# Kernel optimization log

Measured on AMD Instinct MI355X. Metric: run time of the kernel, lower is better.

Reference implementation:

```python
import jax, jax.numpy as jnp
import numpy as np

B, L, D, K, NFFT = 4, 8192, 768, 24, 16384


def setup_inputs() -> dict:
    key = jax.random.key(0)
    k1, k2, k3, k4 = jax.random.split(key, 4)
    x = jax.random.normal(k1, (B, L, D), dtype=jnp.float32)
    phi = jax.random.normal(k2, (L, K), dtype=jnp.float32) * 0.1
    M_inputs = jax.random.normal(k3, (D, D), dtype=jnp.float32) * 0.02
    M_filters = jax.random.normal(k4, (K, D), dtype=jnp.float32) * 0.02
    return {"x": x, "phi": phi, "M_inputs": M_inputs, "M_filters": M_filters, "n": NFFT}


def _convolve_approx(u, v, n):
    # u: (B, L, D) projected inputs; v: (L, D) projected filters (per-channel kernels)
    bsz, seq_len, d = u.shape
    sgn = jnp.where(jnp.arange(seq_len) % 2 == 0, 1.0, -1.0).astype(u.dtype)[None, :, None]  # (1,L,1)
    V = jnp.fft.rfft(v.astype(jnp.float32), n=n, axis=0)[None, :, :, None]  # (1,F,D,1)
    U = jnp.stack([u, u * sgn], axis=-1).astype(jnp.float32)  # (B,L,D,2): [plus, sign-flipped]
    Uf = jnp.fft.rfft(U, n=n, axis=1)  # (B,F,D,2)
    conv = jnp.fft.irfft(V * Uf, n=n, axis=1)[:, :seq_len]  # (B,L,D,2)
    U_plus = conv[..., 0]
    U_minus = conv[..., 1] * sgn
    return U_plus, U_minus


def reference(x, phi, M_inputs, M_filters, n):
    x_proj = x @ M_inputs          # (B,L,D)
    phi_proj = phi @ M_filters     # (L,D)
    spectral_plus, spectral_minus = _convolve_approx(x_proj, phi_proj, n)
    return spectral_plus + spectral_minus
```

## Files before the change

kernel.cpp:

```cpp
#include <hip/hip_runtime.h>
#include <stdint.h>

#define B_SZ 4
#define L_SEQ 8192
#define D_CH 768
#define K_F 24
#define NFFT2 8192
#define LDS_BYTES 69632
#define GEMM_LDS 98304

typedef __attribute__((ext_vector_type(4))) float f32x4;
typedef __attribute__((ext_vector_type(8))) __bf16 bf16x8;

__device__ __forceinline__ uint32_t f2bf1(float f) {
  uint32_t u = __float_as_uint(f);
  return (u + 0x7fffu + ((u >> 16) & 1u)) >> 16;
}
__device__ __forceinline__ uint32_t packbf2(float lo, float hi) {
  return f2bf1(lo) | (f2bf1(hi) << 16);
}
__device__ __forceinline__ float2 unpackbf2(uint32_t v) {
  return float2{__uint_as_float(v << 16), __uint_as_float(v & 0xffff0000u)};
}
__device__ __forceinline__ float2 cmulf(float2 a, float2 b) {
  return float2{a.x * b.x - a.y * b.y, a.x * b.y + a.y * b.x};
}
__device__ __forceinline__ uint32_t pkbf(float lo, float hi) {
  uint32_t r;
  asm("v_cvt_pk_bf16_f32 %0, %1, %2" : "=v"(r) : "v"(lo), "v"(hi));
  return r;
}

__global__ __launch_bounds__(256) void k_mit(const float* __restrict__ Mi,
                                             uint16_t* __restrict__ MiT) {
  int i = blockIdx.x * 256 + threadIdx.x;
  int n = i / 768, e = i - n * 768;
  MiT[i] = (uint16_t)f2bf1(Mi[e * 768 + n]);
}

template <int S>
__device__ __forceinline__ void dft8(float2* x) {
  const float C = 0.70710678118654752f;
  float2 t0{x[0].x + x[4].x, x[0].y + x[4].y}, t1{x[0].x - x[4].x, x[0].y - x[4].y};
  float2 t2{x[2].x + x[6].x, x[2].y + x[6].y}, t3{x[2].x - x[6].x, x[2].y - x[6].y};
  float2 t4{x[1].x + x[5].x, x[1].y + x[5].y}, t5{x[1].x - x[5].x, x[1].y - x[5].y};
  float2 t6{x[3].x + x[7].x, x[3].y + x[7].y}, t7{x[3].x - x[7].x, x[3].y - x[7].y};
  float2 t3r = (S < 0) ? float2{t3.y, -t3.x} : float2{-t3.y, t3.x};
  float2 t7r = (S < 0) ? float2{t7.y, -t7.x} : float2{-t7.y, t7.x};
  float2 e0{t0.x + t2.x, t0.y + t2.y}, e2{t0.x - t2.x, t0.y - t2.y};
  float2 e1{t1.x + t3r.x, t1.y + t3r.y}, e3{t1.x - t3r.x, t1.y - t3r.y};
  float2 o0{t4.x + t6.x, t4.y + t6.y}, o2{t4.x - t6.x, t4.y - t6.y};
  float2 o1{t5.x + t7r.x, t5.y + t7r.y}, o3{t5.x - t7r.x, t5.y - t7r.y};
  float2 o1r = (S < 0) ? float2{C * (o1.x + o1.y), C * (o1.y - o1.x)}
                       : float2{C * (o1.x - o1.y), C * (o1.y + o1.x)};
  float2 o2r = (S < 0) ? float2{o2.y, -o2.x} : float2{-o2.y, o2.x};
  float2 o3r = (S < 0) ? float2{C * (o3.y - o3.x), -C * (o3.x + o3.y)}
                       : float2{-C * (o3.x + o3.y), C * (o3.x - o3.y)};
  x[0] = float2{e0.x + o0.x, e0.y + o0.y};
  x[4] = float2{e0.x - o0.x, e0.y - o0.y};
  x[1] = float2{e1.x + o1r.x, e1.y + o1r.y};
  x[5] = float2{e1.x - o1r.x, e1.y - o1r.y};
  x[2] = float2{e2.x + o2r.x, e2.y + o2r.y};
  x[6] = float2{e2.x - o2r.x, e2.y - o2r.y};
  x[3] = float2{e3.x + o3r.x, e3.y + o3r.y};
  x[7] = float2{e3.x - o3r.x, e3.y - o3r.y};
}

template <int LH, int S, int NT>
__device__ __forceinline__ void pass_r8(float2* a, int tid) {
  constexpr int h = 1 << LH;
  constexpr int st = h + (h >> 4);
  const float ang = (S < 0 ? -6.2831853071795864769f : 6.2831853071795864769f) / (float)(h * 8);
  __syncthreads();
#pragma unroll
  for (int jj = 0; jj < 1024 / NT; ++jj) {
    int j = jj * NT + tid;
    int pos = j & (h - 1);
    int base = ((j >> LH) << (LH + 3)) + pos;
    float2* p = a + (base + (base >> 4));
    float2 x[8];
#pragma unroll
    for (int q = 0; q < 8; ++q) x[q] = p[q * st];
    float sn, cs;
    __sincosf(ang * (float)pos, &sn, &cs);
    float2 w{cs, sn};
    if constexpr (S < 0) {
      dft8<-1>(x);
      float2 wq = w;
      x[1] = cmulf(x[1], wq);
#pragma unroll
      for (int q = 2; q < 8; ++q) {
        wq = cmulf(wq, w);
        x[q] = cmulf(x[q], wq);
      }
    } else {
      float2 wq = w;
      x[1] = cmulf(x[1], wq);
#pragma unroll
      for (int q = 2; q < 8; ++q) {
        wq = cmulf(wq, w);
        x[q] = cmulf(x[q], wq);
      }
      dft8<1>(x);
    }
#pragma unroll
    for (int q = 0; q < 8; ++q) p[q * st] = x[q];
  }
}

__device__ __forceinline__ void p1_fused(float2* a, const uint32_t* __restrict__ row32, int tid) {
#pragma unroll
  for (int jj = 0; jj < 2; ++jj) {
    int j = jj * 512 + tid;
    float2 x[8];
#pragma unroll
    for (int q = 0; q < 4; ++q) x[q] = unpackbf2(row32[j + q * 1024]);
    x[4] = x[5] = x[6] = x[7] = float2{0.f, 0.f};
    dft8<-1>(x);
    float sn, cs;
    __sincosf(-6.2831853071795864769f / 8192.0f * (float)j, &sn, &cs);
    float2 w{cs, sn}, wq = w;
    x[1] = cmulf(x[1], wq);
#pragma unroll
    for (int q = 2; q < 8; ++q) {
      wq = cmulf(wq, w);
      x[q] = cmulf(x[q], wq);
    }
    float2* p = a + (j + (j >> 4));
#pragma unroll
    for (int q = 0; q < 8; ++q) p[q * 1088] = x[q];
  }
}

__device__ __forceinline__ void mid_fused(float2* a, const uint32_t* __restrict__ wrow, int tid) {
  __syncthreads();
#pragma unroll
  for (int jj = 0; jj < 8; ++jj) {
    int j = jj * 512 + tid;
    float2* p = a + (2 * j + ((2 * j) >> 4));
    float2 u = p[0], v = p[1];
    float2 s{u.x + v.x, u.y + v.y}, dd{u.x - v.x, u.y - v.y};
    uint2 wv = *(const uint2*)(wrow + 2 * j);
    s = cmulf(s, unpackbf2(wv.x));
    dd = cmulf(dd, unpackbf2(wv.y));
    p[0] = float2{s.x + dd.x, s.y + dd.y};
    p[1] = float2{s.x - dd.x, s.y - dd.y};
  }
}

__device__ __forceinline__ void last_fused(float2* a, uint32_t* __restrict__ out32, int tid) {
  __syncthreads();
#pragma unroll
  for (int jj = 0; jj < 2; ++jj) {
    int j = jj * 512 + tid;
    float2* p = a + (j + (j >> 4));
    float2 x[8];
#pragma unroll
    for (int q = 0; q < 8; ++q) x[q] = p[q * 1088];
    float sn, cs;
    __sincosf(6.2831853071795864769f / 8192.0f * (float)j, &sn, &cs);
    float2 w{cs, sn}, wq = w;
    x[1] = cmulf(x[1], wq);
#pragma unroll
    for (int q = 2; q < 8; ++q) {
      wq = cmulf(wq, w);
      x[q] = cmulf(x[q], wq);
    }
    dft8<1>(x);
#pragma unroll
    for (int q = 0; q < 4; ++q) out32[j + q * 1024] = packbf2(x[q].x, x[q].y);
  }
}

__global__ __launch_bounds__(256) void k_phi(const float* __restrict__ phi,
                                             float2* __restrict__ Phi2) {
  extern __shared__ float2 buf[];
  int k = blockIdx.x, tid = threadIdx.x;
  const float scale = 2.0f / 8192.0f;
  for (int r = tid; r < 4096; r += 256) {
    buf[r + (r >> 4)] = float2{phi[(2 * r) * K_F + k] * scale, 0.0f};
    int r2i = r + 4096;
    buf[r2i + (r2i >> 4)] = float2{0.0f, 0.0f};
  }
  pass_r8<10, -1, 256>(buf, tid);
  pass_r8<7, -1, 256>(buf, tid);
  pass_r8<4, -1, 256>(buf, tid);
  pass_r8<1, -1, 256>(buf, tid);
  __syncthreads();
  for (int j = tid; j < 4096; j += 256) {
    float2* p = buf + (2 * j + ((2 * j) >> 4));
    float2 u = p[0], v = p[1];
    p[0] = float2{u.x + v.x, u.y + v.y};
    p[1] = float2{u.x - v.x, u.y - v.y};
  }
  __syncthreads();
  for (int f = tid; f < NFFT2; f += 256) Phi2[k * NFFT2 + f] = buf[f + (f >> 4)];
}

__global__ __launch_bounds__(256) void k_w2(const float2* __restrict__ Phi2,
                                            const float* __restrict__ Mf,
                                            uint32_t* __restrict__ W2) {
  __shared__ float2 p[K_F][256];
  __shared__ float mf[K_F][32];
  int tid = threadIdx.x;
  int fc = blockIdx.x & 31, dc = blockIdx.x >> 5;
  int f0 = fc * 256, d0 = dc * 32;
  for (int i = tid; i < K_F * 256; i += 256) {
    int k = i >> 8, fl = i & 255;
    p[k][fl] = Phi2[k * NFFT2 + f0 + fl];
  }
  for (int i = tid; i < K_F * 32; i += 256) {
    int k = i >> 5, dl = i & 31;
    mf[k][dl] = Mf[k * D_CH + d0 + dl];
  }
  __syncthreads();
  for (int dl = 0; dl < 32; ++dl) {
    float re = 0.f, im = 0.f;
#pragma unroll
    for (int k = 0; k < K_F; ++k) {
      float m = mf[k][dl];
      re += m * p[k][tid].x;
      im += m * p[k][tid].y;
    }
    W2[(size_t)(d0 + dl) * NFFT2 + f0 + tid] = packbf2(re, im);
  }
}

__device__ __forceinline__ void gload_lds16(const void* g, void* l) {
  __builtin_amdgcn_global_load_lds(
      (const __attribute__((address_space(1))) void*)g,
      (__attribute__((address_space(3))) void*)l, 16, 0, 0);
}

__global__ __launch_bounds__(512, 2) void k_gemm(const float* __restrict__ X,
                                                 const uint16_t* __restrict__ MiT,
                                                 uint16_t* __restrict__ Cp) {
  extern __shared__ char lds[];
  char* const As0 = lds;
  char* const Bs0 = lds + 32768;
  int tid = threadIdx.x;
  int lane = tid & 63, wid = tid >> 6;
  int p = blockIdx.x;
  int v = (p & 7) * 96 + (p >> 3);
  int bm = v / 3, bn = v % 3;
  int m0 = bm * 128, n0 = bn * 256;
  int wr = wid >> 2, wc = wid & 3;
  int lm = lane & 15, lg = lane >> 4;
  f32x4 acc[4][4] = {};
  float4 fa[4];

#define STAGE_B(bufc, k0)                                              \
  _Pragma("unroll") for (int it = 0; it < 4; ++it) {                   \
    int s = it * 512 + tid;                                            \
    int row = s >> 3;                                                  \
    int cb = ((s & 7) << 4) ^ ((row & 7) << 4);                        \
    gload_lds16(MiT + (size_t)(n0 + row) * 768 + (k0) + (cb >> 1),     \
                Bs0 + (bufc)*32768 + (it * 512 + wid * 64) * 16);      \
  }
#define LOAD_A(k0)                                                     \
  _Pragma("unroll") for (int jt = 0; jt < 2; ++jt) {                   \
    int s = jt * 512 + tid;                                            \
    int row = s >> 3, c16 = s & 7;                                     \
    const float* src = X + (size_t)(m0 + row) * 768 + (k0) + c16 * 8;  \
    fa[2 * jt] = *(const float4*)src;                                  \
    fa[2 * jt + 1] = *(const float4*)(src + 4);                        \
  }
#define WRITE_A(bufc)                                                  \
  _Pragma("unroll") for (int jt = 0; jt < 2; ++jt) {                   \
    int s = jt * 512 + tid;                                            \
    int row = s >> 3, c16 = s & 7;                                     \
    uint4 o;                                                           \
    o.x = pkbf(fa[2 * jt].x, fa[2 * jt].y);                            \
    o.y = pkbf(fa[2 * jt].z, fa[2 * jt].w);                            \
    o.z = pkbf(fa[2 * jt + 1].x, fa[2 * jt + 1].y);                    \
    o.w = pkbf(fa[2 * jt + 1].z, fa[2 * jt + 1].w);                    \
    *(uint4*)(As0 + (bufc)*16384 + row * 128 + ((c16 << 4) ^ ((row & 7) << 4))) = o; \
  }
#define RD_A(dst, bufc, kbyte)                                                         \
  _Pragma("unroll") for (int i = 0; i < 4; ++i) {                                      \
    int row = wr * 64 + i * 16 + lm;                                                   \
    dst[i] = *(const bf16x8*)(As0 + (bufc)*16384 + row * 128 + ((kbyte) ^ ((row & 7) << 4))); \
  }
#define RD_B(dst, bufc, kbyte)                                                         \
  _Pragma("unroll") for (int i = 0; i < 4; ++i) {                                      \
    int row = wc * 64 + i * 16 + lm;                                                   \
    dst[i] = *(const bf16x8*)(Bs0 + (bufc)*32768 + row * 128 + ((kbyte) ^ ((row & 7) << 4))); \
  }
#define MFMA16(av, bv)                                                        \
  _Pragma("unroll") for (int mi = 0; mi < 4; ++mi)                            \
  _Pragma("unroll") for (int ni = 0; ni < 4; ++ni)                            \
      acc[mi][ni] = __builtin_amdgcn_mfma_f32_16x16x32_bf16(av[mi], bv[ni], acc[mi][ni], 0, 0, 0);

  STAGE_B(0, 0);
  LOAD_A(0);
  WRITE_A(0);
  asm volatile("s_waitcnt vmcnt(0) lgkmcnt(0)" ::: "memory");
  __builtin_amdgcn_s_barrier();

  int cur = 0;
  for (int kt = 0; kt < 12; ++kt) {
    int nxt = cur ^ 1, k0n = (kt + 1) * 64;
    int kb0 = lg * 16, kb1 = 64 + lg * 16;
    if (kt < 11) {
      STAGE_B(nxt, k0n);
      LOAD_A(k0n);
    }
    {
      bf16x8 a0[4], b0[4];
      RD_A(a0, cur, kb0);
      RD_B(b0, cur, kb0);
      asm volatile("s_waitcnt lgkmcnt(0)" ::: "memory");
      __builtin_amdgcn_sched_barrier(0);
      __builtin_amdgcn_s_setprio(1);
      MFMA16(a0, b0);
      __builtin_amdgcn_s_setprio(0);
    }
    __builtin_amdgcn_s_barrier();
    {
      bf16x8 a1[4], b1[4];
      RD_A(a1, cur, kb1);
      RD_B(b1, cur, kb1);
      asm volatile("s_waitcnt lgkmcnt(0)" ::: "memory");
      __builtin_amdgcn_sched_barrier(0);
      __builtin_amdgcn_s_setprio(1);
      MFMA16(a1, b1);
      __builtin_amdgcn_s_setprio(0);
    }
    if (kt < 11) WRITE_A(nxt);
    asm volatile("s_waitcnt vmcnt(0) lgkmcnt(0)" ::: "memory");
    __builtin_amdgcn_s_barrier();
    cur = nxt;
  }
#undef STAGE_B
#undef LOAD_A
#undef WRITE_A
#undef RD_A
#undef RD_B
#undef MFMA16

#pragma unroll
  for (int mi = 0; mi < 4; ++mi) {
#pragma unroll
    for (int ni = 0; ni < 4; ++ni) {
      int mg = m0 + wr * 64 + mi * 16 + lg * 4;
      int dd = n0 + wc * 64 + ni * 16 + lm;
      int bb = mg >> 13, t = mg & 8191;
      f32x4 vv = acc[mi][ni];
      uint2 o;
      o.x = packbf2(vv[0], vv[1]);
      o.y = packbf2(vv[2], vv[3]);
      *(uint2*)(Cp + ((size_t)bb * 768 + dd) * 8192 + t) = o;
    }
  }
}

__global__ __launch_bounds__(512, 4) void k_conv(const uint16_t* __restrict__ xprojT,
                                                 const uint32_t* __restrict__ W2,
                                                 uint16_t* __restrict__ convo) {
  extern __shared__ float2 buf[];
  int tid = threadIdx.x;
  int bd = blockIdx.x;
  int d = bd % 768;
  const uint32_t* row32 = (const uint32_t*)(xprojT + (size_t)bd * 8192);
  p1_fused(buf, row32, tid);
  pass_r8<7, -1, 512>(buf, tid);
  pass_r8<4, -1, 512>(buf, tid);
  pass_r8<1, -1, 512>(buf, tid);
  mid_fused(buf, W2 + (size_t)d * NFFT2, tid);
  pass_r8<1, 1, 512>(buf, tid);
  pass_r8<4, 1, 512>(buf, tid);
  pass_r8<7, 1, 512>(buf, tid);
  last_fused(buf, (uint32_t*)(convo + (size_t)bd * 8192), tid);
}

__global__ __launch_bounds__(256) void k_tr(const uint16_t* __restrict__ convo,
                                            float* __restrict__ out) {
  __shared__ uint16_t tile[64][72];
  int tid = threadIdx.x;
  int bx = blockIdx.x;
  int b = bx / 1536;
  int r = bx - b * 1536;
  int d0 = (r >> 7) << 6;
  int t0 = (r & 127) << 6;
  {
    int rr = tid >> 3;
    int c8 = (tid & 7) << 3;
#pragma unroll
    for (int p = 0; p < 2; ++p) {
      int row = p * 32 + rr;
      uint4 v = *(const uint4*)(convo + ((size_t)(b * 768 + d0 + row)) * 8192 + t0 + c8);
      *(uint4*)&tile[row][c8] = v;
    }
  }
  __syncthreads();
  {
    int c4 = (tid & 15) << 2;
    int tg = tid >> 4;
#pragma unroll
    for (int p = 0; p < 4; ++p) {
      int tt = p * 16 + tg;
      float4 o;
      o.x = __uint_as_float((uint32_t)tile[c4 + 0][tt] << 16);
      o.y = __uint_as_float((uint32_t)tile[c4 + 1][tt] << 16);
      o.z = __uint_as_float((uint32_t)tile[c4 + 2][tt] << 16);
      o.w = __uint_as_float((uint32_t)tile[c4 + 3][tt] << 16);
      *(float4*)(out + ((size_t)b * 8192 + t0 + tt) * 768 + d0 + c4) = o;
    }
  }
}

extern "C" void kernel_launch(void* const* d_in, const int* in_sizes, int n_in,
                              void* d_out, int out_size, void* d_ws, size_t ws_size,
                              hipStream_t stream) {
  const float* x   = (const float*)d_in[0];
  const float* phi = (const float*)d_in[1];
  const float* Mi  = (const float*)d_in[2];
  const float* Mf  = (const float*)d_in[3];
  float* out = (float*)d_out;

  uint16_t* xprojT = (uint16_t*)d_out + 25165824;

  char* ws = (char*)d_ws;
  uint16_t* convo = (uint16_t*)ws;
  uint32_t* W2    = (uint32_t*)(ws + 50331648);
  float2*   Phi2  = (float2*)(ws + 75497472);
  uint16_t* MiT   = (uint16_t*)(ws + 77070336);

  k_mit<<<2304, 256, 0, stream>>>(Mi, MiT);
  k_phi<<<24, 256, LDS_BYTES, stream>>>(phi, Phi2);
  k_w2<<<768, 256, 0, stream>>>(Phi2, Mf, W2);
  k_gemm<<<768, 512, GEMM_LDS, stream>>>(x, MiT, xprojT);
  k_conv<<<3072, 512, LDS_BYTES, stream>>>(xprojT, W2, convo);
  k_tr<<<6144, 256, 0, stream>>>(convo, out);
}
```

Baseline: 230.1 us.

## Deepen GEMM prefetch pipeline and fuse last FFT radix stage into pointwise multiply

The GEMM moves to a triple-buffered B stage in LDS and a three-deep register prefetch of A, drops a barrier per k-step and uses partial vmcnt waits, so global loads overlap more with MFMA work. The LDS budget grows to 128KB, which may lower GEMM occupancy. In the conv kernel, the final forward and first inverse radix-8 passes plus the spectral multiply are merged into one in-register radix-16 routine. That removes two LDS passes and barriers per row in exchange for higher register pressure.

```diff
diff --git a/kernel.cpp b/kernel.cpp
--- a/kernel.cpp
+++ b/kernel.cpp
@@ -7,7 +7,7 @@
 #define K_F 24
 #define NFFT2 8192
 #define LDS_BYTES 69632
-#define GEMM_LDS 98304
+#define GEMM_LDS 131072
 
 typedef __attribute__((ext_vector_type(4))) float f32x4;
 typedef __attribute__((ext_vector_type(8))) __bf16 bf16x8;
@@ -132,19 +132,56 @@
   }
 }
 
-__device__ __forceinline__ void mid_fused(float2* a, const uint32_t* __restrict__ wrow, int tid) {
-  __syncthreads();
-#pragma unroll
-  for (int jj = 0; jj < 8; ++jj) {
-    int j = jj * 512 + tid;
-    float2* p = a + (2 * j + ((2 * j) >> 4));
-    float2 u = p[0], v = p[1];
-    float2 s{u.x + v.x, u.y + v.y}, dd{u.x - v.x, u.y - v.y};
-    uint2 wv = *(const uint2*)(wrow + 2 * j);
-    s = cmulf(s, unpackbf2(wv.x));
-    dd = cmulf(dd, unpackbf2(wv.y));
-    p[0] = float2{s.x + dd.x, s.y + dd.y};
-    p[1] = float2{s.x - dd.x, s.y - dd.y};
+__device__ __forceinline__ void mid16(float2* a, const uint32_t* __restrict__ wrow, int tid) {
+  const float C1 = 0.92387953251128675613f, S1 = 0.38268343236508977173f;
+  const float C2 = 0.70710678118654752440f;
+  __syncthreads();
+#pragma unroll
+  for (int jj = 0; jj < 2; ++jj) {
+    int m = jj * 512 + tid;
+    float2* p = a + 17 * m;
+    float2 e[8], o[8];
+#pragma unroll
+    for (int q = 0; q < 8; ++q) {
+      e[q] = p[2 * q];
+      o[q] = p[2 * q + 1];
+    }
+    dft8<-1>(e);
+    dft8<-1>(o);
+    o[1] = cmulf(o[1], float2{C1, -S1});
+    o[2] = cmulf(o[2], float2{C2, -C2});
+    o[3] = cmulf(o[3], float2{S1, -C1});
+    o[4] = float2{o[4].y, -o[4].x};
+    o[5] = cmulf(o[5], float2{-S1, -C1});
+    o[6] = cmulf(o[6], float2{-C2, -C2});
+    o[7] = cmulf(o[7], float2{-C1, -S1});
+    const uint4* wp = (const uint4*)(wrow + 16 * m);
+    uint4 w0 = wp[0], w1 = wp[1], w2 = wp[2], w3 = wp[3];
+    uint32_t wv[16] = {w0.x, w0.y, w0.z, w0.w, w1.x, w1.y, w1.z, w1.w,
+                       w2.x, w2.y, w2.z, w2.w, w3.x, w3.y, w3.z, w3.w};
+#pragma unroll
+    for (int q = 0; q < 8; ++q) {
+      float2 s{e[q].x + o[q].x, e[q].y + o[q].y};
+      float2 d{e[q].x - o[q].x, e[q].y - o[q].y};
+      s = cmulf(s, unpackbf2(wv[2 * q]));
+      d = cmulf(d, unpackbf2(wv[2 * q + 1]));
+      e[q] = float2{s.x + d.x, s.y + d.y};
+      o[q] = float2{s.x - d.x, s.y - d.y};
+    }
+    o[1] = cmulf(o[1], float2{C1, S1});
+    o[2] = cmulf(o[2], float2{C2, C2});
+    o[3] = cmulf(o[3], float2{S1, C1});
+    o[4] = float2{-o[4].y, o[4].x};
+    o[5] = cmulf(o[5], float2{-S1, C1});
+    o[6] = cmulf(o[6], float2{-C2, C2});
+    o[7] = cmulf(o[7], float2{-C1, S1});
+    dft8<1>(e);
+    dft8<1>(o);
+#pragma unroll
+    for (int q = 0; q < 8; ++q) {
+      p[2 * q] = e[q];
+      p[2 * q + 1] = o[q];
+    }
   }
 }
 
@@ -240,14 +277,14 @@
   char* const Bs0 = lds + 32768;
   int tid = threadIdx.x;
   int lane = tid & 63, wid = tid >> 6;
-  int p = blockIdx.x;
-  int v = (p & 7) * 96 + (p >> 3);
+  int pb = blockIdx.x;
+  int v = (pb & 7) * 96 + (pb >> 3);
   int bm = v / 3, bn = v % 3;
   int m0 = bm * 128, n0 = bn * 256;
   int wr = wid >> 2, wc = wid & 3;
   int lm = lane & 15, lg = lane >> 4;
   f32x4 acc[4][4] = {};
-  float4 fa[4];
+  float4 fa[3][4];
 
 #define STAGE_B(bufc, k0)                                              \
   _Pragma("unroll") for (int it = 0; it < 4; ++it) {                   \
@@ -255,36 +292,36 @@
     int row = s >> 3;                                                  \
     int cb = ((s & 7) << 4) ^ ((row & 7) << 4);                        \
     gload_lds16(MiT + (size_t)(n0 + row) * 768 + (k0) + (cb >> 1),     \
-                Bs0 + (bufc)*32768 + (it * 512 + wid * 64) * 16);      \
-  }
-#define LOAD_A(k0)                                                     \
+                Bs0 + (bufc) * 32768 + (it * 512 + wid * 64) * 16);    \
+  }
+#define LOAD_A(aset, k0)                                               \
   _Pragma("unroll") for (int jt = 0; jt < 2; ++jt) {                   \
     int s = jt * 512 + tid;                                            \
     int row = s >> 3, c16 = s & 7;                                     \
     const float* src = X + (size_t)(m0 + row) * 768 + (k0) + c16 * 8;  \
-    fa[2 * jt] = *(const float4*)src;                                  \
-    fa[2 * jt + 1] = *(const float4*)(src + 4);                        \
-  }
-#define WRITE_A(bufc)                                                  \
+    fa[aset][2 * jt] = *(const float4*)src;                            \
+    fa[aset][2 * jt + 1] = *(const float4*)(src + 4);                  \
+  }
+#define WRITE_A(abuf, aset)                                            \
   _Pragma("unroll") for (int jt = 0; jt < 2; ++jt) {                   \
     int s = jt * 512 + tid;                                            \
     int row = s >> 3, c16 = s & 7;                                     \
     uint4 o;                                                           \
-    o.x = pkbf(fa[2 * jt].x, fa[2 * jt].y);                            \
-    o.y = pkbf(fa[2 * jt].z, fa[2 * jt].w);                            \
-    o.z = pkbf(fa[2 * jt + 1].x, fa[2 * jt + 1].y);                    \
-    o.w = pkbf(fa[2 * jt + 1].z, fa[2 * jt + 1].w);                    \
-    *(uint4*)(As0 + (bufc)*16384 + row * 128 + ((c16 << 4) ^ ((row & 7) << 4))) = o; \
-  }
-#define RD_A(dst, bufc, kbyte)                                                         \
-  _Pragma("unroll") for (int i = 0; i < 4; ++i) {                                      \
-    int row = wr * 64 + i * 16 + lm;                                                   \
-    dst[i] = *(const bf16x8*)(As0 + (bufc)*16384 + row * 128 + ((kbyte) ^ ((row & 7) << 4))); \
-  }
-#define RD_B(dst, bufc, kbyte)                                                         \
-  _Pragma("unroll") for (int i = 0; i < 4; ++i) {                                      \
-    int row = wc * 64 + i * 16 + lm;                                                   \
-    dst[i] = *(const bf16x8*)(Bs0 + (bufc)*32768 + row * 128 + ((kbyte) ^ ((row & 7) << 4))); \
+    o.x = pkbf(fa[aset][2 * jt].x, fa[aset][2 * jt].y);                \
+    o.y = pkbf(fa[aset][2 * jt].z, fa[aset][2 * jt].w);                \
+    o.z = pkbf(fa[aset][2 * jt + 1].x, fa[aset][2 * jt + 1].y);        \
+    o.w = pkbf(fa[aset][2 * jt + 1].z, fa[aset][2 * jt + 1].w);        \
+    *(uint4*)(As0 + (abuf) * 16384 + row * 128 + ((c16 << 4) ^ ((row & 7) << 4))) = o; \
+  }
+#define RD_A(dst, abuf, kbyte)                                                              \
+  _Pragma("unroll") for (int i = 0; i < 4; ++i) {                                           \
+    int row = wr * 64 + i * 16 + lm;                                                        \
+    dst[i] = *(const bf16x8*)(As0 + (abuf) * 16384 + row * 128 + ((kbyte) ^ ((row & 7) << 4))); \
+  }
+#define RD_B(dst, bufc, kbyte)                                                              \
+  _Pragma("unroll") for (int i = 0; i < 4; ++i) {                                           \
+    int row = wc * 64 + i * 16 + lm;                                                        \
+    dst[i] = *(const bf16x8*)(Bs0 + (bufc) * 32768 + row * 128 + ((kbyte) ^ ((row & 7) << 4))); \
   }
 #define MFMA16(av, bv)                                                        \
   _Pragma("unroll") for (int mi = 0; mi < 4; ++mi)                            \
@@ -292,44 +329,47 @@
       acc[mi][ni] = __builtin_amdgcn_mfma_f32_16x16x32_bf16(av[mi], bv[ni], acc[mi][ni], 0, 0, 0);
 
   STAGE_B(0, 0);
-  LOAD_A(0);
-  WRITE_A(0);
-  asm volatile("s_waitcnt vmcnt(0) lgkmcnt(0)" ::: "memory");
+  LOAD_A(0, 0);
+  STAGE_B(1, 64);
+  LOAD_A(1, 64);
+  LOAD_A(2, 128);
+  WRITE_A(0, 0);
+  asm volatile("s_waitcnt lgkmcnt(0)" ::: "memory");
   __builtin_amdgcn_s_barrier();
 
-  int cur = 0;
+  int kb0 = lg * 16, kb1 = 64 + lg * 16;
+#pragma unroll
   for (int kt = 0; kt < 12; ++kt) {
-    int nxt = cur ^ 1, k0n = (kt + 1) * 64;
-    int kb0 = lg * 16, kb1 = 64 + lg * 16;
-    if (kt < 11) {
-      STAGE_B(nxt, k0n);
-      LOAD_A(k0n);
-    }
+    if (kt <= 9) STAGE_B((kt + 2) % 3, (kt + 2) * 64);
+    if (kt <= 8) LOAD_A((kt + 3) % 3, (kt + 3) * 64);
     {
       bf16x8 a0[4], b0[4];
-      RD_A(a0, cur, kb0);
-      RD_B(b0, cur, kb0);
+      RD_A(a0, kt & 1, kb0);
+      RD_B(b0, kt % 3, kb0);
       asm volatile("s_waitcnt lgkmcnt(0)" ::: "memory");
       __builtin_amdgcn_sched_barrier(0);
       __builtin_amdgcn_s_setprio(1);
       MFMA16(a0, b0);
       __builtin_amdgcn_s_setprio(0);
     }
-    __builtin_amdgcn_s_barrier();
     {
       bf16x8 a1[4], b1[4];
-      RD_A(a1, cur, kb1);
-      RD_B(b1, cur, kb1);
+      RD_A(a1, kt & 1, kb1);
+      RD_B(b1, kt % 3, kb1);
       asm volatile("s_waitcnt lgkmcnt(0)" ::: "memory");
       __builtin_amdgcn_sched_barrier(0);
       __builtin_amdgcn_s_setprio(1);
       MFMA16(a1, b1);
       __builtin_amdgcn_s_setprio(0);
     }
-    if (kt < 11) WRITE_A(nxt);
-    asm volatile("s_waitcnt vmcnt(0) lgkmcnt(0)" ::: "memory");
-    __builtin_amdgcn_s_barrier();
-    cur = nxt;
+    if (kt <= 10) {
+      WRITE_A((kt + 1) & 1, (kt + 1) % 3);
+      if (kt <= 8)      asm volatile("s_waitcnt vmcnt(12)" ::: "memory");
+      else if (kt == 9) asm volatile("s_waitcnt vmcnt(8)" ::: "memory");
+      else              asm volatile("s_waitcnt vmcnt(0)" ::: "memory");
+      asm volatile("s_waitcnt lgkmcnt(0)" ::: "memory");
+      __builtin_amdgcn_s_barrier();
+    }
   }
 #undef STAGE_B
 #undef LOAD_A
@@ -365,9 +405,7 @@
   p1_fused(buf, row32, tid);
   pass_r8<7, -1, 512>(buf, tid);
   pass_r8<4, -1, 512>(buf, tid);
-  pass_r8<1, -1, 512>(buf, tid);
-  mid_fused(buf, W2 + (size_t)d * NFFT2, tid);
-  pass_r8<1, 1, 512>(buf, tid);
+  mid16(buf, W2 + (size_t)d * NFFT2, tid);
   pass_r8<4, 1, 512>(buf, tid);
   pass_r8<7, 1, 512>(buf, tid);
   last_fused(buf, (uint32_t*)(convo + (size_t)bd * 8192), tid);
```

Result: no change. 234.0 us (+1.7%).
